# Kernel optimization log

Hardware: AMD Instinct MI355X
Metric: run time of the kernel (lower is better)

Reference implementation:

```python
import jax, jax.numpy as jnp
import numpy as np

B, S, D, H, DFF = 4, 2048, 2048, 16, 8192
DH = D // H
THETA = 10000.0
EPS = 1e-5


def rmsnorm(x, g):
    return x * jax.lax.rsqrt(jnp.mean(x * x, axis=-1, keepdims=True) + EPS) * g


def rope(x, pos):
    # x: [B, H, S, DH]; rotate interleaved even/odd pairs
    half = DH // 2
    inv_freq = THETA ** (-(jnp.arange(half, dtype=jnp.float32) * 2.0) / DH)  # [half]
    ang = pos.astype(jnp.float32)[:, None] * inv_freq  # [S, half]
    cos, sin = jnp.cos(ang), jnp.sin(ang)
    x1, x2 = x[..., 0::2], x[..., 1::2]
    r1 = x1 * cos - x2 * sin
    r2 = x1 * sin + x2 * cos
    return jnp.stack([r1, r2], axis=-1).reshape(x.shape)


def setup_inputs() -> dict:
    key = jax.random.key(0)
    ks = jax.random.split(key, 12)
    s = 0.02
    return {
        "x": jax.random.normal(ks[0], (B, S, D), dtype=jnp.float32),
        "attention_mask": jnp.ones((S, S), dtype=bool),
        "wq": jax.random.normal(ks[1], (D, D), dtype=jnp.float32) * s,
        "wk": jax.random.normal(ks[2], (D, D), dtype=jnp.float32) * s,
        "wv": jax.random.normal(ks[3], (D, D), dtype=jnp.float32) * s,
        "wo": jax.random.normal(ks[4], (D, D), dtype=jnp.float32) * s,
        "w1": jax.random.normal(ks[5], (DFF, D), dtype=jnp.float32) * s,
        "w2": jax.random.normal(ks[6], (D, DFF), dtype=jnp.float32) * s,
        "w3": jax.random.normal(ks[7], (DFF, D), dtype=jnp.float32) * s,
        "g1": jnp.ones((D,), dtype=jnp.float32),
        "g2": jnp.ones((D,), dtype=jnp.float32),
    }


def reference(x, attention_mask, wq, wk, wv, wo, w1, w2, w3, g1, g2):
    pos = jnp.arange(x.shape[-2])
    # pre-norm attention
    h = rmsnorm(x, g1)
    q = (h @ wq.T).reshape(B, S, H, DH).transpose(0, 2, 1, 3)
    k = (h @ wk.T).reshape(B, S, H, DH).transpose(0, 2, 1, 3)
    v = (h @ wv.T).reshape(B, S, H, DH).transpose(0, 2, 1, 3)
    q = rope(q, pos)
    k = rope(k, pos)
    scores = jnp.einsum("bhqd,bhkd->bhqk", q, k) / np.float32(np.sqrt(DH))
    scores = jnp.where(attention_mask, scores, jnp.float32(-1e9))
    attn = jax.nn.softmax(scores, axis=-1)
    o = jnp.einsum("bhqk,bhkd->bhqd", attn, v)
    o = o.transpose(0, 2, 1, 3).reshape(B, S, D) @ wo.T
    x = x + o
    # pre-norm SwiGLU FFN
    h2 = rmsnorm(x, g2)
    ffn = (jax.nn.silu(h2 @ w1.T) * (h2 @ w3.T)) @ w2.T
    return x + ffn
```

## Files before the change

kernel.cpp:

```cpp
#include <hip/hip_runtime.h>
#include <cstdint>
#include <cstddef>

#define B_   4
#define S_   2048
#define D_   2048
#define H_   16
#define DH_  128
#define DFF_ 8192
#define LOG2E 1.4426950408889634f

typedef __bf16 bf16_t;
typedef __bf16 bf16x4 __attribute__((ext_vector_type(4)));
typedef __bf16 bf16x8 __attribute__((ext_vector_type(8)));
typedef float  f32x4  __attribute__((ext_vector_type(4)));

#define MFMA16 __builtin_amdgcn_mfma_f32_16x16x32_bf16

__device__ __forceinline__ void glds16(const void* g, void* l) {
  __builtin_amdgcn_global_load_lds((__attribute__((address_space(1))) void*)g,
                                   (__attribute__((address_space(3))) void*)l,
                                   16, 0, 0);
}

__global__ __launch_bounds__(256) void cvt_kernel(const float* __restrict__ in,
                                                  bf16_t* __restrict__ out, int n8) {
  int i = blockIdx.x * 256 + threadIdx.x;
  if (i >= n8) return;
  const float4* p4 = (const float4*)in;
  float4 a = p4[2 * (size_t)i];
  float4 b = p4[2 * (size_t)i + 1];
  bf16x8 o;
  o[0] = (bf16_t)a.x; o[1] = (bf16_t)a.y; o[2] = (bf16_t)a.z; o[3] = (bf16_t)a.w;
  o[4] = (bf16_t)b.x; o[5] = (bf16_t)b.y; o[6] = (bf16_t)b.z; o[7] = (bf16_t)b.w;
  ((bf16x8*)out)[i] = o;
}

__global__ __launch_bounds__(256) void rmsnorm_kernel(const float* __restrict__ x,
                                                      const float* __restrict__ g,
                                                      bf16_t* __restrict__ out) {
  const int row = blockIdx.x, tid = threadIdx.x;
  const float* xr = x + (size_t)row * D_;
  float4 a = ((const float4*)xr)[tid * 2];
  float4 b = ((const float4*)xr)[tid * 2 + 1];
  float ss = a.x*a.x + a.y*a.y + a.z*a.z + a.w*a.w
           + b.x*b.x + b.y*b.y + b.z*b.z + b.w*b.w;
#pragma unroll
  for (int m = 1; m < 64; m <<= 1) ss += __shfl_xor(ss, m);
  __shared__ float red[4];
  if ((tid & 63) == 0) red[tid >> 6] = ss;
  __syncthreads();
  float tot = red[0] + red[1] + red[2] + red[3];
  float rms = rsqrtf(tot * (1.0f / D_) + 1e-5f);
  float4 ga = ((const float4*)g)[tid * 2];
  float4 gb = ((const float4*)g)[tid * 2 + 1];
  bf16x8 o;
  o[0] = (bf16_t)(a.x * rms * ga.x); o[1] = (bf16_t)(a.y * rms * ga.y);
  o[2] = (bf16_t)(a.z * rms * ga.z); o[3] = (bf16_t)(a.w * rms * ga.w);
  o[4] = (bf16_t)(b.x * rms * gb.x); o[5] = (bf16_t)(b.y * rms * gb.y);
  o[6] = (bf16_t)(b.z * rms * gb.z); o[7] = (bf16_t)(b.w * rms * gb.w);
  ((bf16x8*)out)[(size_t)row * 256 + tid] = o;
}


#define Q_RD_A(d, mg)                                                         \
  do {                                                                        \
    const char* p_ = ldsb + (d) * 32768 + (wm * 128 + (mg) * 64 + l15) * 128; \
    _Pragma("unroll") for (int i_ = 0; i_ < 4; i_++) {                        \
      afr[i_][0] = *(const bf16x8*)(p_ + i_ * 2048 + acol0);                  \
      afr[i_][1] = *(const bf16x8*)(p_ + i_ * 2048 + acol1);                  \
    }                                                                         \
  } while (0)

#define Q_RD_B(dst, d, ng)                                                    \
  do {                                                                        \
    const char* p_ = ldsb + 65536 + (d) * 32768 +                             \
                     (wn * 64 + (ng) * 32 + l15) * 128;                       \
    _Pragma("unroll") for (int j_ = 0; j_ < 2; j_++) {                        \
      dst[j_][0] = *(const bf16x8*)(p_ + j_ * 2048 + acol0);                  \
      dst[j_][1] = *(const bf16x8*)(p_ + j_ * 2048 + acol1);                  \
    }                                                                         \
  } while (0)

#define Q_STAGE_A(d, kt)                                                      \
  do {                                                                        \
    char* dst_ = ldsb + (d) * 32768 + o0;                                     \
    const bf16_t* s_ = Asrc + (size_t)(kt) * 64;                              \
    glds16(s_, dst_);                                                         \
    glds16(s_ + 64 * (size_t)K, dst_ + 8192);                                 \
    glds16(s_ + 128 * (size_t)K, dst_ + 16384);                               \
    glds16(s_ + 192 * (size_t)K, dst_ + 24576);                               \
  } while (0)

#define Q_STAGE_B(d, kt)                                                      \
  do {                                                                        \
    char* dst_ = ldsb + 65536 + (d) * 32768 + o0;                             \
    const bf16_t* s_ = Wsrc + (size_t)(kt) * 64;                              \
    glds16(s_, dst_);                                                         \
    glds16(s_ + 64 * (size_t)K, dst_ + 8192);                                 \
    glds16(s_ + 128 * (size_t)K, dst_ + 16384);                               \
    glds16(s_ + 192 * (size_t)K, dst_ + 24576);                               \
  } while (0)

#define Q_MFMA(mg, ng, bsrc)                                                  \
  do {                                                                        \
    __builtin_amdgcn_s_setprio(1);                                            \
    _Pragma("unroll") for (int i_ = 0; i_ < 4; i_++)                          \
    _Pragma("unroll") for (int j_ = 0; j_ < 2; j_++) {                        \
      acc[(mg)*4 + i_][(ng)*2 + j_] =                                         \
          MFMA16(afr[i_][0], bsrc[j_][0], acc[(mg)*4 + i_][(ng)*2 + j_], 0,0,0); \
      acc[(mg)*4 + i_][(ng)*2 + j_] =                                         \
          MFMA16(afr[i_][1], bsrc[j_][1], acc[(mg)*4 + i_][(ng)*2 + j_], 0,0,0); \
    }                                                                         \
    __builtin_amdgcn_s_setprio(0);                                            \
  } while (0)

#define PHASE_FENCE()                                                         \
  do {                                                                        \
    __builtin_amdgcn_sched_barrier(0);                                        \
    __builtin_amdgcn_s_barrier();                                             \
  } while (0)

#define GEMM_EPILOGUE()                                                       \
  _Pragma("unroll") for (int m = 0; m < 8; m++) {                             \
    const int gr = m0 + wm * 128 + m * 16 + lg * 4;                           \
    _Pragma("unroll") for (int nn = 0; nn < 4; nn++) {                        \
      const int gc = n0 + wn * 64 + nn * 16 + l15;                            \
      if constexpr (EPI == 4) {                                               \
        const int seg = gc >> 11;                                             \
        const int gcl = gc & 2047;                                            \
        if (seg < 2) {                                                        \
          bf16_t* o = seg ? outb2 : outb;                                     \
          _Pragma("unroll") for (int r = 0; r < 4; r++)                       \
            o[(size_t)(gr + r) * D_ + gcl] = (bf16_t)acc[m][nn][r];           \
        } else {                                                              \
          const int bb = gr >> 11, ss = gr & 2047;                            \
          bf16x4 pk;                                                          \
          _Pragma("unroll") for (int r = 0; r < 4; r++) pk[r] = (bf16_t)acc[m][nn][r]; \
          *(bf16x4*)(outb3 + ((size_t)bb * D_ + gcl) * S_ + ss) = pk;         \
        }                                                                     \
      } else {                                                                \
        _Pragma("unroll") for (int r = 0; r < 4; r++) {                       \
          size_t idx = (size_t)(gr + r) * N + gc;                             \
          if constexpr (EPI == 0) {                                           \
            outb[idx] = (bf16_t)acc[m][nn][r];                                \
          } else if constexpr (EPI == 1) {                                    \
            outf[idx] = acc[m][nn][r] + addf[idx];                            \
          } else {                                                            \
            float a1v = (float)addb[idx];                                     \
            outb[idx] = (bf16_t)(a1v / (1.0f + expf(-a1v)) * acc[m][nn][r]);  \
          }                                                                   \
        }                                                                     \
      }                                                                       \
    }                                                                         \
  }

#define GEMM_PREAMBLE()                                                       \
  __shared__ char ldsb[131072];                                               \
  const int tid = threadIdx.x;                                                \
  const int wid = tid >> 6, l = tid & 63, l15 = l & 15, lg = l >> 4;          \
  const int wm = wid >> 2, wn = wid & 3;                                      \
  const int nwg = gridDim.x;                                                  \
  int wg = (int)blockIdx.x;                                                   \
  wg = (wg & 7) * (nwg >> 3) + (wg >> 3);                                     \
  const int ntn = N >> 8;                                                     \
  const int ntm = M >> 8;                                                     \
  const int wide = 4 * ntm;                                                   \
  const int grp = wg / wide;                                                  \
  const int rem = wg % wide;                                                  \
  const int m0 = (rem >> 2) << 8;                                             \
  const int n0 = ((grp << 2) + (rem & 3)) << 8;                               \
  f32x4 acc[8][4];                                                            \
  const f32x4 z4 = {0.f, 0.f, 0.f, 0.f};                                      \
  _Pragma("unroll") for (int i = 0; i < 8; i++)                               \
  _Pragma("unroll") for (int j = 0; j < 4; j++) acc[i][j] = z4;               \
  const int o0 = tid * 16;                                                    \
  const int srow = o0 >> 7;                                                   \
  const int ssw = ((o0 & 127) ^ ((srow & 7) << 4)) >> 1;                      \
  const bf16_t* Asrc = A + (size_t)(m0 + srow) * K + ssw;                     \
  const bf16_t* Wsrc = W + (size_t)(n0 + srow) * K + ssw;                     \
  const int rsw = (l15 & 7) << 4;                                             \
  const int acol0 = (lg * 16) ^ rsw;                                          \
  const int acol1 = (64 + lg * 16) ^ rsw;

template <int EPI>
__global__ __launch_bounds__(512, 2) void gemm256(const bf16_t* __restrict__ A,
                                                  const bf16_t* __restrict__ W,
                                                  const float* __restrict__ addf,
                                                  const bf16_t* __restrict__ addb,
                                                  bf16_t* __restrict__ outb,
                                                  bf16_t* __restrict__ outb2,
                                                  bf16_t* __restrict__ outb3,
                                                  float* __restrict__ outf,
                                                  int M, int N, int K) {
  GEMM_PREAMBLE()
  bf16x8 afr[4][2], bfr[2][2];

  const int NT = K >> 6;
  Q_STAGE_A(0, 0);
  Q_STAGE_B(0, 0);
  asm volatile("s_waitcnt vmcnt(0)" ::: "memory");
  __builtin_amdgcn_s_barrier();

  for (int t = 0; t < NT; t++) {
    const int d = t & 1;
    const bool pf = (t + 1 < NT);
    Q_RD_A(d, 0);
    Q_RD_B(bfr, d, 0);
    if (pf) Q_STAGE_A(d ^ 1, t + 1);
    PHASE_FENCE();
    Q_MFMA(0, 0, bfr);
    PHASE_FENCE();
    Q_RD_B(bfr, d, 1);
    if (pf) Q_STAGE_B(d ^ 1, t + 1);
    PHASE_FENCE();
    Q_MFMA(0, 1, bfr);
    PHASE_FENCE();
    Q_RD_A(d, 1);
    PHASE_FENCE();
    Q_MFMA(1, 1, bfr);
    PHASE_FENCE();
    Q_RD_B(bfr, d, 0);
    PHASE_FENCE();
    Q_MFMA(1, 0, bfr);
    asm volatile("s_waitcnt lgkmcnt(0) vmcnt(0)" ::: "memory");
    __builtin_amdgcn_sched_barrier(0);
    __builtin_amdgcn_s_barrier();
  }

  GEMM_EPILOGUE()
}

template <int EPI>
__global__ __launch_bounds__(512, 4) void gemm256h(const bf16_t* __restrict__ A,
                                                   const bf16_t* __restrict__ W,
                                                   const bf16_t* __restrict__ addb,
                                                   bf16_t* __restrict__ outb,
                                                   int M, int N, int K) {
  __shared__ char ldsb[49152];
  const int tid = threadIdx.x;
  const int wid = tid >> 6, l = tid & 63, l15 = l & 15, lg = l >> 4;
  const int wm = wid >> 2, wn = wid & 3;

  const int nwg = gridDim.x;
  int wg = (int)blockIdx.x;
  wg = (wg & 7) * (nwg >> 3) + (wg >> 3);
  const int ntm = M >> 7;
  const int wide = 4 * ntm;
  const int grp = wg / wide;
  const int rem = wg % wide;
  const int m0 = (rem >> 2) << 7;
  const int n0 = ((grp << 2) + (rem & 3)) << 8;

  f32x4 acc[4][4];
  const f32x4 z4 = {0.f, 0.f, 0.f, 0.f};
#pragma unroll
  for (int i = 0; i < 4; i++)
#pragma unroll
    for (int j = 0; j < 4; j++) acc[i][j] = z4;

  const int o0 = tid * 16;
  const int srow = o0 >> 7;
  const int ssw = ((o0 & 127) ^ ((srow & 7) << 4)) >> 1;
  const bf16_t* Asrc = A + (size_t)(m0 + srow) * K + ssw;
  const bf16_t* Wsrc = W + (size_t)(n0 + srow) * K + ssw;
  const int rsw = (l15 & 7) << 4;
  const int acol0 = (lg * 16) ^ rsw;
  const int acol1 = (64 + lg * 16) ^ rsw;

  const int NT = K >> 6;
  for (int t = 0; t < NT; t++) {
    const bf16_t* as = Asrc + (size_t)t * 64;
    glds16(as, ldsb + o0);
    glds16(as + 64 * (size_t)K, ldsb + 8192 + o0);
    const bf16_t* ws = Wsrc + (size_t)t * 64;
    glds16(ws, ldsb + 16384 + o0);
    glds16(ws + 64 * (size_t)K, ldsb + 24576 + o0);
    glds16(ws + 128 * (size_t)K, ldsb + 32768 + o0);
    glds16(ws + 192 * (size_t)K, ldsb + 40960 + o0);
    asm volatile("s_waitcnt vmcnt(0)" ::: "memory");
    __builtin_amdgcn_s_barrier();
    __builtin_amdgcn_sched_barrier(0);
    bf16x8 af[4][2];
#pragma unroll
    for (int fi = 0; fi < 4; fi++) {
      const char* p = ldsb + (wm * 64 + fi * 16 + l15) * 128;
      af[fi][0] = *(const bf16x8*)(p + acol0);
      af[fi][1] = *(const bf16x8*)(p + acol1);
    }
    __builtin_amdgcn_s_setprio(1);
#pragma unroll
    for (int n = 0; n < 4; n++) {
      const char* p = ldsb + 16384 + (wn * 64 + n * 16 + l15) * 128;
      bf16x8 b0 = *(const bf16x8*)(p + acol0);
      bf16x8 b1 = *(const bf16x8*)(p + acol1);
#pragma unroll
      for (int m = 0; m < 4; m++) {
        acc[m][n] = MFMA16(af[m][0], b0, acc[m][n], 0, 0, 0);
        acc[m][n] = MFMA16(af[m][1], b1, acc[m][n], 0, 0, 0);
      }
    }
    __builtin_amdgcn_s_setprio(0);
    __builtin_amdgcn_sched_barrier(0);
    __builtin_amdgcn_s_barrier();
  }

#pragma unroll
  for (int m = 0; m < 4; m++) {
    const int gr = m0 + wm * 64 + m * 16 + lg * 4;
#pragma unroll
    for (int n = 0; n < 4; n++) {
      const int gc = n0 + wn * 64 + n * 16 + l15;
#pragma unroll
      for (int r = 0; r < 4; r++) {
        size_t idx = (size_t)(gr + r) * N + gc;
        if constexpr (EPI == 0) {
          outb[idx] = (bf16_t)acc[m][n][r];
        } else {
          float a1v = (float)addb[idx];
          outb[idx] = (bf16_t)(a1v / (1.0f + expf(-a1v)) * acc[m][n][r]);
        }
      }
    }
  }
}

__global__ __launch_bounds__(256) void rope_kernel(bf16_t* __restrict__ buf) {
  size_t i = (size_t)blockIdx.x * 256 + threadIdx.x;
  int pi = (int)(i & 63);
  size_t rh = i >> 6;
  int srow = (int)((rh / H_) % S_);
  float inv = expf((float)pi * (-9.210340371976184f / 64.0f));
  float ang = (float)srow * inv;
  float c = cosf(ang), sn = sinf(ang);
  bf16_t* p = buf + i * 2;
  float x1 = (float)p[0], x2 = (float)p[1];
  p[0] = (bf16_t)(x1 * c - x2 * sn);
  p[1] = (bf16_t)(x1 * sn + x2 * c);
}

__global__ __launch_bounds__(256) void attn_kernel(const bf16_t* __restrict__ Q,
                                                   const bf16_t* __restrict__ Kb,
                                                   const bf16_t* __restrict__ Vt,
                                                   bf16_t* __restrict__ O) {
  const int qt = blockIdx.x, h = blockIdx.y, b = blockIdx.z;
  const int tid = threadIdx.x;
  const int wid = tid >> 6, l = tid & 63, l15 = l & 15, lg = l >> 4;

  __shared__ bf16_t Klds[64 * 128];
  __shared__ bf16_t Vlds[128 * 64];
  __shared__ bf16_t Plds[4][16 * 72];

  const int q0 = qt * 64 + wid * 16;
  const f32x4 z4 = {0.f, 0.f, 0.f, 0.f};

  bf16x8 qf[4];
  {
    const bf16_t* qp = Q + ((size_t)(b * S_ + q0 + l15)) * D_ + h * DH_ + lg * 8;
#pragma unroll
    for (int kk = 0; kk < 4; kk++) qf[kk] = *(const bf16x8*)(qp + kk * 32);
  }
  f32x4 of[8];
#pragma unroll
  for (int f = 0; f < 8; f++) of[f] = z4;
  float m_run = -1e30f, l_run = 0.f;

  const int o0 = tid * 16;
  const int krow0 = o0 >> 8;
  const int scol = ((o0 & 255) ^ ((krow0 & 7) << 4)) >> 1;
  const int vrow0 = o0 >> 7;
  const int vcol = ((o0 & 127) ^ ((vrow0 & 7) << 4)) >> 1;

  const size_t bh_off = ((size_t)b * S_) * D_ + (size_t)h * DH_;
  const bf16_t* vtbase = Vt + ((size_t)b * D_ + h * DH_) * S_;

  for (int kv0 = 0; kv0 < S_; kv0 += 64) {
    const bf16_t* kbase = Kb + bh_off + (size_t)kv0 * D_;
#pragma unroll
    for (int s = 0; s < 4; s++)
      glds16(kbase + (size_t)(krow0 + 16 * s) * D_ + scol,
             (char*)Klds + s * 4096 + wid * 1024);
#pragma unroll
    for (int s = 0; s < 4; s++)
      glds16(vtbase + (size_t)(vrow0 + 32 * s) * S_ + kv0 + vcol,
             (char*)Vlds + s * 4096 + wid * 1024);
    __syncthreads();

    f32x4 st[4];
#pragma unroll
    for (int c = 0; c < 4; c++) {
      st[c] = z4;
      const int row = c * 16 + l15;
      const char* kr = (const char*)Klds + row * 256;
      const int sw = (row & 7) << 4;
#pragma unroll
      for (int kk = 0; kk < 4; kk++) {
        bf16x8 kf = *(const bf16x8*)(kr + ((kk * 64 + lg * 16) ^ sw));
        st[c] = MFMA16(kf, qf[kk], st[c], 0, 0, 0);
      }
    }

    float s[16];
#pragma unroll
    for (int c = 0; c < 4; c++)
#pragma unroll
      for (int r = 0; r < 4; r++) s[c * 4 + r] = st[c][r] * 0.08838834764831845f;
    float pm = s[0];
#pragma unroll
    for (int i = 1; i < 16; i++) pm = fmaxf(pm, s[i]);
    pm = fmaxf(pm, __shfl_xor(pm, 16));
    pm = fmaxf(pm, __shfl_xor(pm, 32));
    float mnew = fmaxf(m_run, pm);
    float alpha = exp2f((m_run - mnew) * LOG2E);
    float p[16], ts = 0.f;
#pragma unroll
    for (int i = 0; i < 16; i++) { p[i] = exp2f((s[i] - mnew) * LOG2E); ts += p[i]; }
    ts += __shfl_xor(ts, 16);
    ts += __shfl_xor(ts, 32);
    l_run = l_run * alpha + ts;
    m_run = mnew;

    float aq[4];
#pragma unroll
    for (int r = 0; r < 4; r++) aq[r] = __shfl(alpha, lg * 4 + r);
#pragma unroll
    for (int f = 0; f < 8; f++)
#pragma unroll
      for (int r = 0; r < 4; r++) of[f][r] *= aq[r];

    bf16_t* pw = &Plds[wid][0];
#pragma unroll
    for (int c = 0; c < 4; c++)
#pragma unroll
      for (int r = 0; r < 4; r++)
        pw[l15 * 72 + c * 16 + lg * 4 + r] = (bf16_t)p[c * 4 + r];
    asm volatile("s_waitcnt lgkmcnt(0)" ::: "memory");
    bf16x8 pa0 = *(const bf16x8*)(pw + l15 * 72 + lg * 8);
    bf16x8 pa1 = *(const bf16x8*)(pw + l15 * 72 + 32 + lg * 8);
#pragma unroll
    for (int f = 0; f < 8; f++) {
      const int row = 16 * f + l15;
      const char* vr = (const char*)Vlds + row * 128;
      const int sw = (row & 7) << 4;
      bf16x8 bv0 = *(const bf16x8*)(vr + ((lg * 16) ^ sw));
      bf16x8 bv1 = *(const bf16x8*)(vr + ((64 + lg * 16) ^ sw));
      of[f] = MFMA16(pa0, bv0, of[f], 0, 0, 0);
      of[f] = MFMA16(pa1, bv1, of[f], 0, 0, 0);
    }
    __syncthreads();
  }

  float inv[4];
#pragma unroll
  for (int r = 0; r < 4; r++) inv[r] = 1.0f / __shfl(l_run, lg * 4 + r);
#pragma unroll
  for (int f = 0; f < 8; f++)
#pragma unroll
    for (int r = 0; r < 4; r++)
      O[((size_t)(b * S_ + q0 + lg * 4 + r)) * D_ + h * DH_ + 16 * f + l15] =
          (bf16_t)(of[f][r] * inv[r]);
}

extern "C" void kernel_launch(void* const* d_in, const int* in_sizes, int n_in,
                              void* d_out, int out_size, void* d_ws, size_t ws_size,
                              hipStream_t stream) {
  const float* x  = (const float*)d_in[0];
  const float* wq = (const float*)d_in[2];
  const float* wk = (const float*)d_in[3];
  const float* wv = (const float*)d_in[4];
  const float* wo = (const float*)d_in[5];
  const float* w1 = (const float*)d_in[6];
  const float* w2 = (const float*)d_in[7];
  const float* w3 = (const float*)d_in[8];
  const float* g1 = (const float*)d_in[9];
  const float* g2 = (const float*)d_in[10];
  float* out = (float*)d_out;

  const size_t ND = (size_t)D_ * D_;
  const size_t NF = (size_t)DFF_ * D_;
  const size_t SLOT = NF * 2;
  char* base = (char*)d_ws;
  bf16_t* wslot = (bf16_t*)(base);
  bf16_t* h1    = (bf16_t*)(base + 1 * SLOT);
  bf16_t* qb    = (bf16_t*)(base + 2 * SLOT);
  bf16_t* kb    = (bf16_t*)(base + 3 * SLOT);
  bf16_t* vt    = (bf16_t*)(base + 4 * SLOT);
  bf16_t* ob    = (bf16_t*)(base + 5 * SLOT);
  bf16_t* h2    = h1;
  bf16_t* g     = qb;
  float*  x1    = out;

  auto cvt = [&](const float* in, bf16_t* o, size_t n) {
    int n8 = (int)(n / 8);
    cvt_kernel<<<(n8 + 255) / 256, 256, 0, stream>>>(in, o, n8);
  };

  rmsnorm_kernel<<<B_ * S_, 256, 0, stream>>>(x, g1, h1);

  cvt(wq, wslot, ND);
  cvt(wk, wslot + ND, ND);
  cvt(wv, wslot + 2 * ND, ND);
  const int gqkv3 = (8192 / 256) * (6144 / 256);
  gemm256<4><<<gqkv3, 512, 0, stream>>>(h1, wslot, nullptr, nullptr,
                                        qb, kb, vt, nullptr, 8192, 6144, 2048);

  rope_kernel<<<(B_ * S_ * H_ * 64) / 256, 256, 0, stream>>>(qb);
  rope_kernel<<<(B_ * S_ * H_ * 64) / 256, 256, 0, stream>>>(kb);

  dim3 ga(S_ / 64, H_, B_);
  attn_kernel<<<ga, 256, 0, stream>>>(qb, kb, vt, ob);

  const int gqkv = (8192 / 256) * (2048 / 256);
  cvt(wo, wslot, ND);
  gemm256<1><<<gqkv, 512, 0, stream>>>(ob, wslot, x, nullptr,
                                       nullptr, nullptr, nullptr, x1, 8192, 2048, 2048);

  rmsnorm_kernel<<<B_ * S_, 256, 0, stream>>>(x1, g2, h2);

  const int gffh = (8192 / 128) * (8192 / 256);
  cvt(w1, wslot, NF);
  gemm256h<0><<<gffh, 512, 0, stream>>>(h2, wslot, nullptr, g, 8192, 8192, 2048);

  cvt(w3, wslot, NF);
  gemm256h<2><<<gffh, 512, 0, stream>>>(h2, wslot, g, g, 8192, 8192, 2048);

  cvt(w2, wslot, NF);
  gemm256<1><<<gqkv, 512, 0, stream>>>(g, wslot, x1, nullptr,
                                       nullptr, nullptr, nullptr, x1, 8192, 2048, 8192);
}
```

Measured before the change: 1.436 ms.

## Route all GEMMs through 128x256 tile kernel and add lazy softmax rescaling

Removes the 256x256 gemm256 kernel and generalizes the 128x256 gemm256h kernel with all epilogue variants (QKV split with V transpose, residual add), so the QKV, output-projection and down-projection GEMMs run on smaller tiles with higher occupancy and more workgroups. In attention, the scale is folded with log2e, and the running max/output rescale is skipped unless some row's max grows by more than 8 (in log2 units). This cuts exp and multiply work per KV tile. The cost is more tile reloads from the smaller tiles, plus unnormalized exponentials up to 2^8, which lowers precision margin in bf16 P.

```diff
diff --git a/kernel.cpp b/kernel.cpp
--- a/kernel.cpp
+++ b/kernel.cpp
@@ -62,180 +62,15 @@
   ((bf16x8*)out)[(size_t)row * 256 + tid] = o;
 }
 
-
-#define Q_RD_A(d, mg)                                                         \
-  do {                                                                        \
-    const char* p_ = ldsb + (d) * 32768 + (wm * 128 + (mg) * 64 + l15) * 128; \
-    _Pragma("unroll") for (int i_ = 0; i_ < 4; i_++) {                        \
-      afr[i_][0] = *(const bf16x8*)(p_ + i_ * 2048 + acol0);                  \
-      afr[i_][1] = *(const bf16x8*)(p_ + i_ * 2048 + acol1);                  \
-    }                                                                         \
-  } while (0)
-
-#define Q_RD_B(dst, d, ng)                                                    \
-  do {                                                                        \
-    const char* p_ = ldsb + 65536 + (d) * 32768 +                             \
-                     (wn * 64 + (ng) * 32 + l15) * 128;                       \
-    _Pragma("unroll") for (int j_ = 0; j_ < 2; j_++) {                        \
-      dst[j_][0] = *(const bf16x8*)(p_ + j_ * 2048 + acol0);                  \
-      dst[j_][1] = *(const bf16x8*)(p_ + j_ * 2048 + acol1);                  \
-    }                                                                         \
-  } while (0)
-
-#define Q_STAGE_A(d, kt)                                                      \
-  do {                                                                        \
-    char* dst_ = ldsb + (d) * 32768 + o0;                                     \
-    const bf16_t* s_ = Asrc + (size_t)(kt) * 64;                              \
-    glds16(s_, dst_);                                                         \
-    glds16(s_ + 64 * (size_t)K, dst_ + 8192);                                 \
-    glds16(s_ + 128 * (size_t)K, dst_ + 16384);                               \
-    glds16(s_ + 192 * (size_t)K, dst_ + 24576);                               \
-  } while (0)
-
-#define Q_STAGE_B(d, kt)                                                      \
-  do {                                                                        \
-    char* dst_ = ldsb + 65536 + (d) * 32768 + o0;                             \
-    const bf16_t* s_ = Wsrc + (size_t)(kt) * 64;                              \
-    glds16(s_, dst_);                                                         \
-    glds16(s_ + 64 * (size_t)K, dst_ + 8192);                                 \
-    glds16(s_ + 128 * (size_t)K, dst_ + 16384);                               \
-    glds16(s_ + 192 * (size_t)K, dst_ + 24576);                               \
-  } while (0)
-
-#define Q_MFMA(mg, ng, bsrc)                                                  \
-  do {                                                                        \
-    __builtin_amdgcn_s_setprio(1);                                            \
-    _Pragma("unroll") for (int i_ = 0; i_ < 4; i_++)                          \
-    _Pragma("unroll") for (int j_ = 0; j_ < 2; j_++) {                        \
-      acc[(mg)*4 + i_][(ng)*2 + j_] =                                         \
-          MFMA16(afr[i_][0], bsrc[j_][0], acc[(mg)*4 + i_][(ng)*2 + j_], 0,0,0); \
-      acc[(mg)*4 + i_][(ng)*2 + j_] =                                         \
-          MFMA16(afr[i_][1], bsrc[j_][1], acc[(mg)*4 + i_][(ng)*2 + j_], 0,0,0); \
-    }                                                                         \
-    __builtin_amdgcn_s_setprio(0);                                            \
-  } while (0)
-
-#define PHASE_FENCE()                                                         \
-  do {                                                                        \
-    __builtin_amdgcn_sched_barrier(0);                                        \
-    __builtin_amdgcn_s_barrier();                                             \
-  } while (0)
-
-#define GEMM_EPILOGUE()                                                       \
-  _Pragma("unroll") for (int m = 0; m < 8; m++) {                             \
-    const int gr = m0 + wm * 128 + m * 16 + lg * 4;                           \
-    _Pragma("unroll") for (int nn = 0; nn < 4; nn++) {                        \
-      const int gc = n0 + wn * 64 + nn * 16 + l15;                            \
-      if constexpr (EPI == 4) {                                               \
-        const int seg = gc >> 11;                                             \
-        const int gcl = gc & 2047;                                            \
-        if (seg < 2) {                                                        \
-          bf16_t* o = seg ? outb2 : outb;                                     \
-          _Pragma("unroll") for (int r = 0; r < 4; r++)                       \
-            o[(size_t)(gr + r) * D_ + gcl] = (bf16_t)acc[m][nn][r];           \
-        } else {                                                              \
-          const int bb = gr >> 11, ss = gr & 2047;                            \
-          bf16x4 pk;                                                          \
-          _Pragma("unroll") for (int r = 0; r < 4; r++) pk[r] = (bf16_t)acc[m][nn][r]; \
-          *(bf16x4*)(outb3 + ((size_t)bb * D_ + gcl) * S_ + ss) = pk;         \
-        }                                                                     \
-      } else {                                                                \
-        _Pragma("unroll") for (int r = 0; r < 4; r++) {                       \
-          size_t idx = (size_t)(gr + r) * N + gc;                             \
-          if constexpr (EPI == 0) {                                           \
-            outb[idx] = (bf16_t)acc[m][nn][r];                                \
-          } else if constexpr (EPI == 1) {                                    \
-            outf[idx] = acc[m][nn][r] + addf[idx];                            \
-          } else {                                                            \
-            float a1v = (float)addb[idx];                                     \
-            outb[idx] = (bf16_t)(a1v / (1.0f + expf(-a1v)) * acc[m][nn][r]);  \
-          }                                                                   \
-        }                                                                     \
-      }                                                                       \
-    }                                                                         \
-  }
-
-#define GEMM_PREAMBLE()                                                       \
-  __shared__ char ldsb[131072];                                               \
-  const int tid = threadIdx.x;                                                \
-  const int wid = tid >> 6, l = tid & 63, l15 = l & 15, lg = l >> 4;          \
-  const int wm = wid >> 2, wn = wid & 3;                                      \
-  const int nwg = gridDim.x;                                                  \
-  int wg = (int)blockIdx.x;                                                   \
-  wg = (wg & 7) * (nwg >> 3) + (wg >> 3);                                     \
-  const int ntn = N >> 8;                                                     \
-  const int ntm = M >> 8;                                                     \
-  const int wide = 4 * ntm;                                                   \
-  const int grp = wg / wide;                                                  \
-  const int rem = wg % wide;                                                  \
-  const int m0 = (rem >> 2) << 8;                                             \
-  const int n0 = ((grp << 2) + (rem & 3)) << 8;                               \
-  f32x4 acc[8][4];                                                            \
-  const f32x4 z4 = {0.f, 0.f, 0.f, 0.f};                                      \
-  _Pragma("unroll") for (int i = 0; i < 8; i++)                               \
-  _Pragma("unroll") for (int j = 0; j < 4; j++) acc[i][j] = z4;               \
-  const int o0 = tid * 16;                                                    \
-  const int srow = o0 >> 7;                                                   \
-  const int ssw = ((o0 & 127) ^ ((srow & 7) << 4)) >> 1;                      \
-  const bf16_t* Asrc = A + (size_t)(m0 + srow) * K + ssw;                     \
-  const bf16_t* Wsrc = W + (size_t)(n0 + srow) * K + ssw;                     \
-  const int rsw = (l15 & 7) << 4;                                             \
-  const int acol0 = (lg * 16) ^ rsw;                                          \
-  const int acol1 = (64 + lg * 16) ^ rsw;
-
-template <int EPI>
-__global__ __launch_bounds__(512, 2) void gemm256(const bf16_t* __restrict__ A,
-                                                  const bf16_t* __restrict__ W,
-                                                  const float* __restrict__ addf,
-                                                  const bf16_t* __restrict__ addb,
-                                                  bf16_t* __restrict__ outb,
-                                                  bf16_t* __restrict__ outb2,
-                                                  bf16_t* __restrict__ outb3,
-                                                  float* __restrict__ outf,
-                                                  int M, int N, int K) {
-  GEMM_PREAMBLE()
-  bf16x8 afr[4][2], bfr[2][2];
-
-  const int NT = K >> 6;
-  Q_STAGE_A(0, 0);
-  Q_STAGE_B(0, 0);
-  asm volatile("s_waitcnt vmcnt(0)" ::: "memory");
-  __builtin_amdgcn_s_barrier();
-
-  for (int t = 0; t < NT; t++) {
-    const int d = t & 1;
-    const bool pf = (t + 1 < NT);
-    Q_RD_A(d, 0);
-    Q_RD_B(bfr, d, 0);
-    if (pf) Q_STAGE_A(d ^ 1, t + 1);
-    PHASE_FENCE();
-    Q_MFMA(0, 0, bfr);
-    PHASE_FENCE();
-    Q_RD_B(bfr, d, 1);
-    if (pf) Q_STAGE_B(d ^ 1, t + 1);
-    PHASE_FENCE();
-    Q_MFMA(0, 1, bfr);
-    PHASE_FENCE();
-    Q_RD_A(d, 1);
-    PHASE_FENCE();
-    Q_MFMA(1, 1, bfr);
-    PHASE_FENCE();
-    Q_RD_B(bfr, d, 0);
-    PHASE_FENCE();
-    Q_MFMA(1, 0, bfr);
-    asm volatile("s_waitcnt lgkmcnt(0) vmcnt(0)" ::: "memory");
-    __builtin_amdgcn_sched_barrier(0);
-    __builtin_amdgcn_s_barrier();
-  }
-
-  GEMM_EPILOGUE()
-}
-
 template <int EPI>
 __global__ __launch_bounds__(512, 4) void gemm256h(const bf16_t* __restrict__ A,
                                                    const bf16_t* __restrict__ W,
+                                                   const float* __restrict__ addf,
                                                    const bf16_t* __restrict__ addb,
                                                    bf16_t* __restrict__ outb,
+                                                   bf16_t* __restrict__ outb2,
+                                                   bf16_t* __restrict__ outb3,
+                                                   float* __restrict__ outf,
                                                    int M, int N, int K) {
   __shared__ char ldsb[49152];
   const int tid = threadIdx.x;
@@ -311,14 +146,33 @@
 #pragma unroll
     for (int n = 0; n < 4; n++) {
       const int gc = n0 + wn * 64 + n * 16 + l15;
-#pragma unroll
-      for (int r = 0; r < 4; r++) {
-        size_t idx = (size_t)(gr + r) * N + gc;
-        if constexpr (EPI == 0) {
-          outb[idx] = (bf16_t)acc[m][n][r];
+      if constexpr (EPI == 4) {
+        const int seg = gc >> 11;
+        const int gcl = gc & 2047;
+        if (seg < 2) {
+          bf16_t* o = seg ? outb2 : outb;
+#pragma unroll
+          for (int r = 0; r < 4; r++)
+            o[(size_t)(gr + r) * D_ + gcl] = (bf16_t)acc[m][n][r];
         } else {
-          float a1v = (float)addb[idx];
-          outb[idx] = (bf16_t)(a1v / (1.0f + expf(-a1v)) * acc[m][n][r]);
+          const int bb = gr >> 11, ss = gr & 2047;
+          bf16x4 pk;
+#pragma unroll
+          for (int r = 0; r < 4; r++) pk[r] = (bf16_t)acc[m][n][r];
+          *(bf16x4*)(outb3 + ((size_t)bb * D_ + gcl) * S_ + ss) = pk;
+        }
+      } else {
+#pragma unroll
+        for (int r = 0; r < 4; r++) {
+          size_t idx = (size_t)(gr + r) * N + gc;
+          if constexpr (EPI == 0) {
+            outb[idx] = (bf16_t)acc[m][n][r];
+          } else if constexpr (EPI == 1) {
+            outf[idx] = acc[m][n][r] + addf[idx];
+          } else {
+            float a1v = (float)addb[idx];
+            outb[idx] = (bf16_t)(a1v / (1.0f + expf(-a1v)) * acc[m][n][r]);
+          }
         }
       }
     }
@@ -353,6 +207,7 @@
 
   const int q0 = qt * 64 + wid * 16;
   const f32x4 z4 = {0.f, 0.f, 0.f, 0.f};
+  const float SCL = 0.08838834764831845f * LOG2E;
 
   bf16x8 qf[4];
   {
@@ -404,29 +259,31 @@
 #pragma unroll
     for (int c = 0; c < 4; c++)
 #pragma unroll
-      for (int r = 0; r < 4; r++) s[c * 4 + r] = st[c][r] * 0.08838834764831845f;
+      for (int r = 0; r < 4; r++) s[c * 4 + r] = st[c][r] * SCL;
     float pm = s[0];
 #pragma unroll
     for (int i = 1; i < 16; i++) pm = fmaxf(pm, s[i]);
     pm = fmaxf(pm, __shfl_xor(pm, 16));
     pm = fmaxf(pm, __shfl_xor(pm, 32));
-    float mnew = fmaxf(m_run, pm);
-    float alpha = exp2f((m_run - mnew) * LOG2E);
+    if (!__all(pm - m_run <= 8.0f)) {
+      float mnew = fmaxf(m_run, pm);
+      float alpha = exp2f(m_run - mnew);
+      float aq[4];
+#pragma unroll
+      for (int r = 0; r < 4; r++) aq[r] = __shfl(alpha, lg * 4 + r);
+#pragma unroll
+      for (int f = 0; f < 8; f++)
+#pragma unroll
+        for (int r = 0; r < 4; r++) of[f][r] *= aq[r];
+      l_run *= alpha;
+      m_run = mnew;
+    }
     float p[16], ts = 0.f;
 #pragma unroll
-    for (int i = 0; i < 16; i++) { p[i] = exp2f((s[i] - mnew) * LOG2E); ts += p[i]; }
+    for (int i = 0; i < 16; i++) { p[i] = exp2f(s[i] - m_run); ts += p[i]; }
     ts += __shfl_xor(ts, 16);
     ts += __shfl_xor(ts, 32);
-    l_run = l_run * alpha + ts;
-    m_run = mnew;
-
-    float aq[4];
-#pragma unroll
-    for (int r = 0; r < 4; r++) aq[r] = __shfl(alpha, lg * 4 + r);
-#pragma unroll
-    for (int f = 0; f < 8; f++)
-#pragma unroll
-      for (int r = 0; r < 4; r++) of[f][r] *= aq[r];
+    l_run += ts;
 
     bf16_t* pw = &Plds[wid][0];
 #pragma unroll
@@ -500,9 +357,9 @@
   cvt(wq, wslot, ND);
   cvt(wk, wslot + ND, ND);
   cvt(wv, wslot + 2 * ND, ND);
-  const int gqkv3 = (8192 / 256) * (6144 / 256);
-  gemm256<4><<<gqkv3, 512, 0, stream>>>(h1, wslot, nullptr, nullptr,
-                                        qb, kb, vt, nullptr, 8192, 6144, 2048);
+  const int gqkv3 = (8192 / 128) * (6144 / 256);
+  gemm256h<4><<<gqkv3, 512, 0, stream>>>(h1, wslot, nullptr, nullptr,
+                                         qb, kb, vt, nullptr, 8192, 6144, 2048);
 
   rope_kernel<<<(B_ * S_ * H_ * 64) / 256, 256, 0, stream>>>(qb);
   rope_kernel<<<(B_ * S_ * H_ * 64) / 256, 256, 0, stream>>>(kb);
@@ -510,21 +367,23 @@
   dim3 ga(S_ / 64, H_, B_);
   attn_kernel<<<ga, 256, 0, stream>>>(qb, kb, vt, ob);
 
-  const int gqkv = (8192 / 256) * (2048 / 256);
+  const int gd = (8192 / 128) * (2048 / 256);
   cvt(wo, wslot, ND);
-  gemm256<1><<<gqkv, 512, 0, stream>>>(ob, wslot, x, nullptr,
-                                       nullptr, nullptr, nullptr, x1, 8192, 2048, 2048);
+  gemm256h<1><<<gd, 512, 0, stream>>>(ob, wslot, x, nullptr,
+                                      nullptr, nullptr, nullptr, x1, 8192, 2048, 2048);
 
   rmsnorm_kernel<<<B_ * S_, 256, 0, stream>>>(x1, g2, h2);
 
   const int gffh = (8192 / 128) * (8192 / 256);
   cvt(w1, wslot, NF);
-  gemm256h<0><<<gffh, 512, 0, stream>>>(h2, wslot, nullptr, g, 8192, 8192, 2048);
+  gemm256h<0><<<gffh, 512, 0, stream>>>(h2, wslot, nullptr, nullptr,
+                                        g, nullptr, nullptr, nullptr, 8192, 8192, 2048);
 
   cvt(w3, wslot, NF);
-  gemm256h<2><<<gffh, 512, 0, stream>>>(h2, wslot, g, g, 8192, 8192, 2048);
+  gemm256h<2><<<gffh, 512, 0, stream>>>(h2, wslot, nullptr, g,
+                                        g, nullptr, nullptr, nullptr, 8192, 8192, 2048);
 
   cvt(w2, wslot, NF);
-  gemm256<1><<<gqkv, 512, 0, stream>>>(g, wslot, x1, nullptr,
-                                       nullptr, nullptr, nullptr, x1, 8192, 2048, 8192);
-}
+  gemm256h<1><<<gd, 512, 0, stream>>>(g, wslot, x1, nullptr,
+                                      nullptr, nullptr, nullptr, x1, 8192, 2048, 8192);
+}
```

After: 1.405 ms. -2.2%, faster.
